# Optimization experiments

Measured on AMD Instinct MI355X. Metric: run time of the kernel, lower is better.

The kernel has to match this reference:

```python
import jax, jax.numpy as jnp
import numpy as np

N = 50000      # nodes
E = 800000     # edges (avg degree 16)
F = 128        # num_features
H = 64         # nhid
S = 3          # num_scatter


def setup_inputs() -> dict:
    key = jax.random.key(0)
    ks = jax.random.split(key, 10)
    x = jax.random.normal(ks[0], (N, F), dtype=jnp.float32)
    scatter_edge_index = jax.random.randint(ks[1], (2, E), 0, N, dtype=jnp.int32)
    scatter_edge_attr = jax.random.normal(ks[2], (E,), dtype=jnp.float32)
    s = 0.05
    lin_W = jax.random.normal(ks[3], (F, H), dtype=jnp.float32) * s
    lin_b = jnp.zeros((H,), dtype=jnp.float32)
    # per-scatter-block 2-layer MLP applied after edge aggregation (layer=2)
    W1 = jax.random.normal(ks[4], (S, H, H), dtype=jnp.float32) * s
    b1 = jnp.zeros((S, H), dtype=jnp.float32)
    W2 = jax.random.normal(ks[5], (S, H, H), dtype=jnp.float32) * s
    b2 = jnp.zeros((S, H), dtype=jnp.float32)
    return {
        'x': x,
        'scatter_edge_index': scatter_edge_index,
        'scatter_edge_attr': scatter_edge_attr,
        'lin_W': lin_W, 'lin_b': lin_b,
        'W1': W1, 'b1': b1, 'W2': W2, 'b2': b2,
    }


def reference(x, scatter_edge_index, scatter_edge_attr, lin_W, lin_b, W1, b1, W2, b2):
    src = scatter_edge_index[0]
    dst = scatter_edge_index[1]
    attr = scatter_edge_attr[:, None]  # [E,1]

    def conv(h, i):
        # gather -> edge-weight -> scatter-add (message passing), then 2-layer MLP
        m = jax.ops.segment_sum(h[src] * attr, dst, num_segments=N)  # [N,H]
        t = jax.nn.relu(m @ W1[i] + b1[i])
        return t @ W2[i] + b2[i]

    h = x @ lin_W + lin_b  # lin_in (dropout is identity at eval)
    outs, scats = [], []
    for i in range(S):
        h = h + conv(h, i)          # residual accumulation
        outs.append(h)
        scats.append(conv(h, i))    # second conv on updated hidden_rep
    return (jnp.stack(scats), jnp.stack(outs))  # ([S,N,H], [S,N,H])
```

## Files before the change

kernel.cpp:

```cpp
#include <hip/hip_runtime.h>

#define NN 50000
#define NE 800000
#define FIN 128
#define HD 64
#define SL 3
#define GBM 782
#define NBIN 196
#define BSH 8
#define CAP 8064

typedef __attribute__((ext_vector_type(8))) short bf16x8;
typedef __attribute__((ext_vector_type(4))) float f32x4;
#define MFMA(A, B, C) __builtin_amdgcn_mfma_f32_16x16x32_bf16(A, B, C, 0, 0, 0)


__device__ __forceinline__ unsigned int bfr(float x) {
    unsigned int u = __float_as_uint(x);
    return (u + 0x7fffu + ((u >> 16) & 1u)) >> 16;
}
__device__ __forceinline__ unsigned int bf2(float lo, float hi) {
    return bfr(lo) | (bfr(hi) << 16);
}


__global__ void zero_k(int* __restrict__ g) {
    if (threadIdx.x < NBIN) g[threadIdx.x] = 0;
}

__global__ __launch_bounds__(256) void binpass_k(const int* __restrict__ src,
                                                 const int* __restrict__ dst,
                                                 const float* __restrict__ attr,
                                                 int* __restrict__ gcur,
                                                 int2* __restrict__ tedge) {
    __shared__ int cnt_lds[256], runbase[256], lcur[256];
    int t = threadIdx.x;
    cnt_lds[t] = 0;
    lcur[t] = 0;
    __syncthreads();
    int base = blockIdx.x * 4096;
    for (int i = t; i < 4096; i += 256) {
        int e = base + i;
        if (e < NE) atomicAdd(&cnt_lds[dst[e] >> BSH], 1);
    }
    __syncthreads();
    if (t < NBIN && cnt_lds[t]) runbase[t] = atomicAdd(&gcur[t], cnt_lds[t]);
    __syncthreads();
    for (int i = t; i < 4096; i += 256) {
        int e = base + i;
        if (e < NE) {
            int d = dst[e];
            int b = d >> BSH;
            int r = atomicAdd(&lcur[b], 1);
            tedge[(size_t)b * CAP + runbase[b] + r] =
                make_int2(src[e] | ((d & 255) << 16), __float_as_int(attr[e]));
        }
    }
}

__global__ __launch_bounds__(256) void binscan_k(const int* __restrict__ gcur,
                                                 int* __restrict__ binoff,
                                                 int* __restrict__ off) {
    __shared__ int sh[256];
    int t = threadIdx.x;
    int v = (t < NBIN) ? gcur[t] : 0;
    sh[t] = v;
    __syncthreads();
    for (int d = 1; d < 256; d <<= 1) {
        int u = (t >= d) ? sh[t - d] : 0;
        __syncthreads();
        sh[t] += u;
        __syncthreads();
    }
    if (t < NBIN) binoff[t] = sh[t] - v;
    if (t == 255) {
        binoff[NBIN] = sh[255];
        off[NN] = sh[255];
    }
}

__global__ __launch_bounds__(256) void sortbin2_k(const int* __restrict__ binoff,
                                                  const int2* __restrict__ tedge,
                                                  int2* __restrict__ cedge,
                                                  int* __restrict__ off) {
    __shared__ int cnt[256], lofs[256], lcur[256];
    int b = blockIdx.x, t = threadIdx.x;
    int s = binoff[b];
    int n_in_bin = binoff[b + 1] - s;
    const int2* tb = tedge + (size_t)b * CAP;
    cnt[t] = 0;
    __syncthreads();
    for (int i = t; i < n_in_bin; i += 256)
        atomicAdd(&cnt[((unsigned)tb[i].x >> 16) & 255], 1);
    __syncthreads();
    int v = cnt[t];
    lofs[t] = v;
    __syncthreads();
    for (int d = 1; d < 256; d <<= 1) {
        int u = (t >= d) ? lofs[t - d] : 0;
        __syncthreads();
        lofs[t] += u;
        __syncthreads();
    }
    int ex = lofs[t] - v;
    int node = (b << BSH) + t;
    if (node < NN) off[node] = s + ex;
    lcur[t] = ex;
    __syncthreads();
    for (int i = t; i < n_in_bin; i += 256) {
        int2 ed = tb[i];
        int dl = ((unsigned)ed.x >> 16) & 255;
        int p = s + atomicAdd(&lcur[dl], 1);
        cedge[p] = make_int2(ed.x & 0xffff, ed.y);
    }
}


__global__ __launch_bounds__(256) void wprep_k(const float* __restrict__ W1,
                                               const float* __restrict__ W2,
                                               const float* __restrict__ linW,
                                               short* __restrict__ prep) {
    int i = blockIdx.x * 256 + threadIdx.x;
    if (i < 24576) {
        int mat = i >> 12;
        int o = i & 4095;
        int j = o & 7, l = (o >> 3) & 63, s = (o >> 9) & 1, t = o >> 10;
        int k = 32 * s + 8 * (l >> 4) + j;
        int n = 16 * t + (l & 15);
        const float* Wsrc = (mat & 1) ? W2 : W1;
        prep[i] = (short)bfr(Wsrc[(mat >> 1) * 4096 + k * 64 + n]);
    } else if (i < 32768) {
        int o = i - 24576;
        int j = o & 7, l = (o >> 3) & 63, s = (o >> 9) & 3, t = o >> 11;
        int k = 32 * s + 8 * (l >> 4) + j;
        int n = 16 * t + (l & 15);
        prep[i] = (short)bfr(linW[k * 64 + n]);
    }
}


__global__ __launch_bounds__(256) void scatter_k(const uint4* __restrict__ hb4,
                                                 const int* __restrict__ off,
                                                 const int2* __restrict__ cedge,
                                                 uint4* __restrict__ mb4) {
    int w    = (blockIdx.x * blockDim.x + threadIdx.x) >> 6;
    int lane = threadIdx.x & 63;
    if (w >= NN) return;
    int g = lane >> 3;
    int f = lane & 7;
    int s = off[w], e = off[w + 1];
    float a0 = 0.f, a1 = 0.f, a2 = 0.f, a3 = 0.f;
    float a4 = 0.f, a5 = 0.f, a6 = 0.f, a7 = 0.f;
    for (int i = s + g; i < e; i += 8) {
        int2 ed = cedge[i];
        uint4 hv = hb4[(size_t)ed.x * 8 + f];
        float a = __int_as_float(ed.y);
        a0 += a * __uint_as_float(hv.x << 16);
        a1 += a * __uint_as_float(hv.x & 0xffff0000u);
        a2 += a * __uint_as_float(hv.y << 16);
        a3 += a * __uint_as_float(hv.y & 0xffff0000u);
        a4 += a * __uint_as_float(hv.z << 16);
        a5 += a * __uint_as_float(hv.z & 0xffff0000u);
        a6 += a * __uint_as_float(hv.w << 16);
        a7 += a * __uint_as_float(hv.w & 0xffff0000u);
    }
#pragma unroll
    for (int msk = 8; msk <= 32; msk <<= 1) {
        a0 += __shfl_xor(a0, msk);
        a1 += __shfl_xor(a1, msk);
        a2 += __shfl_xor(a2, msk);
        a3 += __shfl_xor(a3, msk);
        a4 += __shfl_xor(a4, msk);
        a5 += __shfl_xor(a5, msk);
        a6 += __shfl_xor(a6, msk);
        a7 += __shfl_xor(a7, msk);
    }
    if (g == 0) {
        uint4 o;
        o.x = bf2(a0, a1);
        o.y = bf2(a2, a3);
        o.z = bf2(a4, a5);
        o.w = bf2(a6, a7);
        mb4[(size_t)w * 8 + f] = o;
    }
}


__device__ __forceinline__ void conv_core(bf16x8 a0, bf16x8 a1,
                                          const bf16x8* __restrict__ w1f,
                                          const float* __restrict__ b1,
                                          const bf16x8* __restrict__ w2f,
                                          short* tw, int c, int q, int l,
                                          f32x4 oc[4]) {
    f32x4 acc[4];
#pragma unroll
    for (int t = 0; t < 4; t++) acc[t] = (f32x4){0.f, 0.f, 0.f, 0.f};
#pragma unroll
    for (int t = 0; t < 4; t++) {
        acc[t] = MFMA(a0, w1f[(t * 2 + 0) * 64 + l], acc[t]);
        acc[t] = MFMA(a1, w1f[(t * 2 + 1) * 64 + l], acc[t]);
    }
#pragma unroll
    for (int t = 0; t < 4; t++) {
        float bb = b1[16 * t + c];
#pragma unroll
        for (int rg = 0; rg < 4; rg++) {
            float v = fmaxf(acc[t][rg] + bb, 0.f);
            tw[(4 * q + rg) * 72 + 16 * t + c] = (short)bfr(v);
        }
    }
    __syncthreads();
    bf16x8 ta0 = *(const bf16x8*)&tw[c * 72 + 8 * q];
    bf16x8 ta1 = *(const bf16x8*)&tw[c * 72 + 32 + 8 * q];
#pragma unroll
    for (int t = 0; t < 4; t++) oc[t] = (f32x4){0.f, 0.f, 0.f, 0.f};
#pragma unroll
    for (int t = 0; t < 4; t++) {
        oc[t] = MFMA(ta0, w2f[(t * 2 + 0) * 64 + l], oc[t]);
        oc[t] = MFMA(ta1, w2f[(t * 2 + 1) * 64 + l], oc[t]);
    }
}


template <bool ADD, bool WB>
__global__ __launch_bounds__(256) void convm_k(const unsigned int* __restrict__ mb,
                                               const short* __restrict__ w1p,
                                               const float* __restrict__ b1,
                                               const short* __restrict__ w2p,
                                               const float* __restrict__ b2,
                                               const float* __restrict__ hprev,
                                               float* __restrict__ out,
                                               unsigned int* __restrict__ hb) {
    __shared__ short tls[4][16 * 72];
    int wv = threadIdx.x >> 6, l = threadIdx.x & 63;
    int c = l & 15, q = l >> 4;
    int rbase = blockIdx.x * 64 + wv * 16;

    int ar = rbase + c;
    bool aok = ar < NN;
    uint4 v0 = make_uint4(0, 0, 0, 0), v1 = v0;
    if (aok) {
        const uint4* mp = (const uint4*)(mb + (size_t)ar * 32);
        v0 = mp[q];
        v1 = mp[4 + q];
    }
    bf16x8 a0 = *(bf16x8*)&v0, a1 = *(bf16x8*)&v1;

    f32x4 oc[4];
    conv_core(a0, a1, (const bf16x8*)w1p, b1, (const bf16x8*)w2p, tls[wv], c, q, l, oc);

#pragma unroll
    for (int t = 0; t < 4; t++) {
        float bb = b2[16 * t + c];
#pragma unroll
        for (int rg = 0; rg < 4; rg++) {
            int row = rbase + 4 * q + rg;
            if (row < NN) {
                float v = oc[t][rg] + bb;
                if constexpr (ADD) v += hprev[(size_t)row * 64 + 16 * t + c];
                out[(size_t)row * 64 + 16 * t + c] = v;
                if constexpr (WB) {
                    float o = __shfl_xor(v, 1);
                    if ((c & 1) == 0)
                        hb[(size_t)row * 32 + 8 * t + (c >> 1)] = bf2(v, o);
                }
            }
        }
    }
}


__global__ __launch_bounds__(256) void conv2_k(const unsigned int* __restrict__ mb,
                                               const short* __restrict__ wa1,
                                               const float* __restrict__ ba1,
                                               const short* __restrict__ wa2,
                                               const float* __restrict__ ba2,
                                               const short* __restrict__ wb1,
                                               const float* __restrict__ bb1,
                                               const short* __restrict__ wb2,
                                               const float* __restrict__ bb2,
                                               const float* __restrict__ hprev,
                                               float* __restrict__ outa,
                                               float* __restrict__ outb,
                                               unsigned int* __restrict__ hb) {
    __shared__ short tls[4][16 * 72];
    int wv = threadIdx.x >> 6, l = threadIdx.x & 63;
    int c = l & 15, q = l >> 4;
    int rbase = blockIdx.x * 64 + wv * 16;

    int ar = rbase + c;
    bool aok = ar < NN;
    uint4 v0 = make_uint4(0, 0, 0, 0), v1 = v0;
    if (aok) {
        const uint4* mp = (const uint4*)(mb + (size_t)ar * 32);
        v0 = mp[q];
        v1 = mp[4 + q];
    }
    bf16x8 a0 = *(bf16x8*)&v0, a1 = *(bf16x8*)&v1;

    f32x4 oc[4];
    conv_core(a0, a1, (const bf16x8*)wa1, ba1, (const bf16x8*)wa2, tls[wv], c, q, l, oc);
#pragma unroll
    for (int t = 0; t < 4; t++) {
        float bb = ba2[16 * t + c];
#pragma unroll
        for (int rg = 0; rg < 4; rg++) {
            int row = rbase + 4 * q + rg;
            if (row < NN)
                outa[(size_t)row * 64 + 16 * t + c] = oc[t][rg] + bb;
        }
    }
    __syncthreads();

    conv_core(a0, a1, (const bf16x8*)wb1, bb1, (const bf16x8*)wb2, tls[wv], c, q, l, oc);
#pragma unroll
    for (int t = 0; t < 4; t++) {
        float bb = bb2[16 * t + c];
#pragma unroll
        for (int rg = 0; rg < 4; rg++) {
            int row = rbase + 4 * q + rg;
            if (row < NN) {
                float v = oc[t][rg] + bb + hprev[(size_t)row * 64 + 16 * t + c];
                outb[(size_t)row * 64 + 16 * t + c] = v;
                float o = __shfl_xor(v, 1);
                if ((c & 1) == 0)
                    hb[(size_t)row * 32 + 8 * t + (c >> 1)] = bf2(v, o);
            }
        }
    }
}


__global__ __launch_bounds__(256) void linm_k(const float* __restrict__ x,
                                              const short* __restrict__ wp,
                                              const float* __restrict__ b,
                                              float* __restrict__ h0,
                                              unsigned int* __restrict__ hb) {
    int wv = threadIdx.x >> 6, l = threadIdx.x & 63;
    int c = l & 15, q = l >> 4;
    int rbase = blockIdx.x * 64 + wv * 16;
    int ar = rbase + c;
    bool aok = ar < NN;

    bf16x8 af[4];
#pragma unroll
    for (int s = 0; s < 4; s++) {
        float4 p0 = make_float4(0, 0, 0, 0), p1 = p0;
        if (aok) {
            const float4* xp = (const float4*)(x + (size_t)ar * FIN + 32 * s + 8 * q);
            p0 = xp[0];
            p1 = xp[1];
        }
        bf16x8 t;
        t[0] = (short)bfr(p0.x); t[1] = (short)bfr(p0.y);
        t[2] = (short)bfr(p0.z); t[3] = (short)bfr(p0.w);
        t[4] = (short)bfr(p1.x); t[5] = (short)bfr(p1.y);
        t[6] = (short)bfr(p1.z); t[7] = (short)bfr(p1.w);
        af[s] = t;
    }

    const bf16x8* wf = (const bf16x8*)wp;
    f32x4 acc[4];
#pragma unroll
    for (int t = 0; t < 4; t++) acc[t] = (f32x4){0.f, 0.f, 0.f, 0.f};
#pragma unroll
    for (int t = 0; t < 4; t++)
#pragma unroll
        for (int s = 0; s < 4; s++)
            acc[t] = MFMA(af[s], wf[(t * 4 + s) * 64 + l], acc[t]);

#pragma unroll
    for (int t = 0; t < 4; t++) {
        float bb = b[16 * t + c];
#pragma unroll
        for (int rg = 0; rg < 4; rg++) {
            int row = rbase + 4 * q + rg;
            if (row < NN) {
                float v = acc[t][rg] + bb;
                h0[(size_t)row * 64 + 16 * t + c] = v;
                float o = __shfl_xor(v, 1);
                if ((c & 1) == 0)
                    hb[(size_t)row * 32 + 8 * t + (c >> 1)] = bf2(v, o);
            }
        }
    }
}


extern "C" void kernel_launch(void* const* d_in, const int* in_sizes, int n_in,
                              void* d_out, int out_size, void* d_ws, size_t ws_size,
                              hipStream_t stream) {
    (void)in_sizes; (void)n_in; (void)out_size; (void)ws_size;

    const float* x    = (const float*)d_in[0];
    const int*   ei   = (const int*)d_in[1];
    const float* attr = (const float*)d_in[2];
    const float* linW = (const float*)d_in[3];
    const float* linb = (const float*)d_in[4];
    const float* W1   = (const float*)d_in[5];
    const float* b1   = (const float*)d_in[6];
    const float* W2   = (const float*)d_in[7];
    const float* b2   = (const float*)d_in[8];
    float* out = (float*)d_out;

    float*        h0     = (float*)d_ws;
    unsigned int* mb     = (unsigned int*)(h0 + (size_t)NN * HD);
    unsigned int* hb     = mb + (size_t)NN * 32;
    int2*         cedge  = (int2*)(hb + (size_t)NN * 32);
    short*        prep   = (short*)(cedge + NE);
    int*          off    = (int*)(prep + 32768);
    int*          gcur   = off + NN + 1;
    int*          binoff = gcur + 256;
    int2*         tedge  = (int2*)h0;

    const int* src = ei;
    const int* dst = ei + NE;

    float* scats = out;
    float* outs  = out + (size_t)SL * NN * HD;

    const size_t NH = (size_t)NN * HD;
    const int WB_ = (NN * 64) / 256;

    const short* w1p0 = prep;
    const short* w2p0 = prep + 4096;
    const short* linp = prep + 24576;

    zero_k<<<1, 256, 0, stream>>>(gcur);
    binpass_k<<<196, 256, 0, stream>>>(src, dst, attr, gcur, tedge);
    binscan_k<<<1, 256, 0, stream>>>(gcur, binoff, off);
    sortbin2_k<<<NBIN, 256, 0, stream>>>(binoff, tedge, cedge, off);
    wprep_k<<<128, 256, 0, stream>>>(W1, W2, linW, prep);

    linm_k<<<GBM, 256, 0, stream>>>(x, linp, linb, h0, hb);

    scatter_k<<<WB_, 256, 0, stream>>>((const uint4*)hb, off, cedge, (uint4*)mb);
    convm_k<true, true><<<GBM, 256, 0, stream>>>(mb, w1p0, b1, w2p0, b2, h0, outs, hb);

    scatter_k<<<WB_, 256, 0, stream>>>((const uint4*)hb, off, cedge, (uint4*)mb);
    conv2_k<<<GBM, 256, 0, stream>>>(mb, w1p0, b1, w2p0, b2,
                                     w1p0 + 8192, b1 + 64, w2p0 + 8192, b2 + 64,
                                     outs, scats, outs + NH, hb);

    scatter_k<<<WB_, 256, 0, stream>>>((const uint4*)hb, off, cedge, (uint4*)mb);
    conv2_k<<<GBM, 256, 0, stream>>>(mb, w1p0 + 8192, b1 + 64, w2p0 + 8192, b2 + 64,
                                     w1p0 + 16384, b1 + 128, w2p0 + 16384, b2 + 128,
                                     outs + NH, scats + NH, outs + 2 * NH, hb);

    scatter_k<<<WB_, 256, 0, stream>>>((const uint4*)hb, off, cedge, (uint4*)mb);
    convm_k<false, false><<<GBM, 256, 0, stream>>>(mb, w1p0 + 16384, b1 + 128,
                                                   w2p0 + 16384, b2 + 128,
                                                   nullptr, scats + 2 * NH, nullptr);
}
```

Baseline: 209.2 us.

## Split bf16 hidden features into two feature-half arrays and merge sort/prep kernels

Result: slower. 257.8 us (+23.3%).

```diff
diff --git a/kernel.cpp b/kernel.cpp
--- a/kernel.cpp
+++ b/kernel.cpp
@@ -9,6 +9,7 @@
 #define NBIN 196
 #define BSH 8
 #define CAP 8064
+#define SCB 25000
 
 typedef __attribute__((ext_vector_type(8))) short bf16x8;
 typedef __attribute__((ext_vector_type(4))) float f32x4;
@@ -58,11 +59,36 @@
     }
 }
 
-__global__ __launch_bounds__(256) void binscan_k(const int* __restrict__ gcur,
-                                                 int* __restrict__ binoff,
-                                                 int* __restrict__ off) {
-    __shared__ int sh[256];
+__global__ __launch_bounds__(256) void sortprep_k(const int* __restrict__ gcur,
+                                                  const int2* __restrict__ tedge,
+                                                  int2* __restrict__ cedge,
+                                                  int* __restrict__ off,
+                                                  const float* __restrict__ W1,
+                                                  const float* __restrict__ W2,
+                                                  const float* __restrict__ linW,
+                                                  short* __restrict__ prep) {
     int t = threadIdx.x;
+    if (blockIdx.x >= NBIN) {
+        int i = (blockIdx.x - NBIN) * 256 + t;
+        if (i < 24576) {
+            int mat = i >> 12;
+            int o = i & 4095;
+            int j = o & 7, l = (o >> 3) & 63, s = (o >> 9) & 1, tt = o >> 10;
+            int k = 32 * s + 8 * (l >> 4) + j;
+            int n = 16 * tt + (l & 15);
+            const float* Wsrc = (mat & 1) ? W2 : W1;
+            prep[i] = (short)bfr(Wsrc[(mat >> 1) * 4096 + k * 64 + n]);
+        } else if (i < 32768) {
+            int o = i - 24576;
+            int j = o & 7, l = (o >> 3) & 63, s = (o >> 9) & 3, tt = o >> 11;
+            int k = 32 * s + 8 * (l >> 4) + j;
+            int n = 16 * tt + (l & 15);
+            prep[i] = (short)bfr(linW[k * 64 + n]);
+        }
+        return;
+    }
+    __shared__ int sh[256], cnt[256], lofs[256], lcur[256];
+    int b = blockIdx.x;
     int v = (t < NBIN) ? gcur[t] : 0;
     sh[t] = v;
     __syncthreads();
@@ -72,29 +98,18 @@
         sh[t] += u;
         __syncthreads();
     }
-    if (t < NBIN) binoff[t] = sh[t] - v;
-    if (t == 255) {
-        binoff[NBIN] = sh[255];
-        off[NN] = sh[255];
-    }
-}
-
-__global__ __launch_bounds__(256) void sortbin2_k(const int* __restrict__ binoff,
-                                                  const int2* __restrict__ tedge,
-                                                  int2* __restrict__ cedge,
-                                                  int* __restrict__ off) {
-    __shared__ int cnt[256], lofs[256], lcur[256];
-    int b = blockIdx.x, t = threadIdx.x;
-    int s = binoff[b];
-    int n_in_bin = binoff[b + 1] - s;
+    int s = (b == 0) ? 0 : sh[b - 1];
+    int n_in_bin = sh[b] - s;
+    if (b == NBIN - 1 && t == 0) off[NN] = sh[NBIN - 1];
+
     const int2* tb = tedge + (size_t)b * CAP;
     cnt[t] = 0;
     __syncthreads();
     for (int i = t; i < n_in_bin; i += 256)
         atomicAdd(&cnt[((unsigned)tb[i].x >> 16) & 255], 1);
     __syncthreads();
-    int v = cnt[t];
-    lofs[t] = v;
+    int cv = cnt[t];
+    lofs[t] = cv;
     __syncthreads();
     for (int d = 1; d < 256; d <<= 1) {
         int u = (t >= d) ? lofs[t - d] : 0;
@@ -102,7 +117,7 @@
         lofs[t] += u;
         __syncthreads();
     }
-    int ex = lofs[t] - v;
+    int ex = lofs[t] - cv;
     int node = (b << BSH) + t;
     if (node < NN) off[node] = s + ex;
     lcur[t] = ex;
@@ -116,44 +131,26 @@
 }
 
 
-__global__ __launch_bounds__(256) void wprep_k(const float* __restrict__ W1,
-                                               const float* __restrict__ W2,
-                                               const float* __restrict__ linW,
-                                               short* __restrict__ prep) {
-    int i = blockIdx.x * 256 + threadIdx.x;
-    if (i < 24576) {
-        int mat = i >> 12;
-        int o = i & 4095;
-        int j = o & 7, l = (o >> 3) & 63, s = (o >> 9) & 1, t = o >> 10;
-        int k = 32 * s + 8 * (l >> 4) + j;
-        int n = 16 * t + (l & 15);
-        const float* Wsrc = (mat & 1) ? W2 : W1;
-        prep[i] = (short)bfr(Wsrc[(mat >> 1) * 4096 + k * 64 + n]);
-    } else if (i < 32768) {
-        int o = i - 24576;
-        int j = o & 7, l = (o >> 3) & 63, s = (o >> 9) & 3, t = o >> 11;
-        int k = 32 * s + 8 * (l >> 4) + j;
-        int n = 16 * t + (l & 15);
-        prep[i] = (short)bfr(linW[k * 64 + n]);
-    }
-}
-
-
-__global__ __launch_bounds__(256) void scatter_k(const uint4* __restrict__ hb4,
+__global__ __launch_bounds__(256) void scatter_k(const uint4* __restrict__ hbL,
+                                                 const uint4* __restrict__ hbH,
                                                  const int* __restrict__ off,
                                                  const int2* __restrict__ cedge,
-                                                 uint4* __restrict__ mb4) {
-    int w    = (blockIdx.x * blockDim.x + threadIdx.x) >> 6;
+                                                 uint4* __restrict__ mbL,
+                                                 uint4* __restrict__ mbH) {
+    int gid = blockIdx.x * 4 + (int)(threadIdx.x >> 6);
+    int half = gid >= NN;
+    int w = half ? gid - NN : gid;
+    const uint4* hb4 = half ? hbH : hbL;
+    uint4* mb4 = half ? mbH : mbL;
     int lane = threadIdx.x & 63;
-    if (w >= NN) return;
-    int g = lane >> 3;
-    int f = lane & 7;
+    int g = lane >> 2;
+    int f = lane & 3;
     int s = off[w], e = off[w + 1];
     float a0 = 0.f, a1 = 0.f, a2 = 0.f, a3 = 0.f;
     float a4 = 0.f, a5 = 0.f, a6 = 0.f, a7 = 0.f;
-    for (int i = s + g; i < e; i += 8) {
+    for (int i = s + g; i < e; i += 16) {
         int2 ed = cedge[i];
-        uint4 hv = hb4[(size_t)ed.x * 8 + f];
+        uint4 hv = hb4[(size_t)ed.x * 4 + f];
         float a = __int_as_float(ed.y);
         a0 += a * __uint_as_float(hv.x << 16);
         a1 += a * __uint_as_float(hv.x & 0xffff0000u);
@@ -165,7 +162,7 @@
         a7 += a * __uint_as_float(hv.w & 0xffff0000u);
     }
 #pragma unroll
-    for (int msk = 8; msk <= 32; msk <<= 1) {
+    for (int msk = 4; msk <= 32; msk <<= 1) {
         a0 += __shfl_xor(a0, msk);
         a1 += __shfl_xor(a1, msk);
         a2 += __shfl_xor(a2, msk);
@@ -181,7 +178,7 @@
         o.y = bf2(a2, a3);
         o.z = bf2(a4, a5);
         o.w = bf2(a6, a7);
-        mb4[(size_t)w * 8 + f] = o;
+        mb4[(size_t)w * 4 + f] = o;
     }
 }
 
@@ -222,29 +219,48 @@
 }
 
 
+__device__ __forceinline__ void load_afrag(const uint4* __restrict__ mbL,
+                                           const uint4* __restrict__ mbH,
+                                           int ar, int q, bf16x8& a0, bf16x8& a1) {
+    uint4 v0 = make_uint4(0, 0, 0, 0), v1 = v0;
+    if (ar < NN) {
+        v0 = mbL[(size_t)ar * 4 + q];
+        v1 = mbH[(size_t)ar * 4 + q];
+    }
+    a0 = *(bf16x8*)&v0;
+    a1 = *(bf16x8*)&v1;
+}
+
+
+__device__ __forceinline__ void wb_hb(unsigned int* __restrict__ hbL,
+                                      unsigned int* __restrict__ hbH,
+                                      int row, int t, int c, float v) {
+    float o = __shfl_xor(v, 1);
+    if ((c & 1) == 0) {
+        unsigned int* hx = (t < 2) ? hbL : hbH;
+        hx[(size_t)row * 16 + 8 * (t & 1) + (c >> 1)] = bf2(v, o);
+    }
+}
+
+
 template <bool ADD, bool WB>
-__global__ __launch_bounds__(256) void convm_k(const unsigned int* __restrict__ mb,
+__global__ __launch_bounds__(256) void convm_k(const uint4* __restrict__ mbL,
+                                               const uint4* __restrict__ mbH,
                                                const short* __restrict__ w1p,
                                                const float* __restrict__ b1,
                                                const short* __restrict__ w2p,
                                                const float* __restrict__ b2,
                                                const float* __restrict__ hprev,
                                                float* __restrict__ out,
-                                               unsigned int* __restrict__ hb) {
+                                               unsigned int* __restrict__ hbL,
+                                               unsigned int* __restrict__ hbH) {
     __shared__ short tls[4][16 * 72];
     int wv = threadIdx.x >> 6, l = threadIdx.x & 63;
     int c = l & 15, q = l >> 4;
     int rbase = blockIdx.x * 64 + wv * 16;
 
-    int ar = rbase + c;
-    bool aok = ar < NN;
-    uint4 v0 = make_uint4(0, 0, 0, 0), v1 = v0;
-    if (aok) {
-        const uint4* mp = (const uint4*)(mb + (size_t)ar * 32);
-        v0 = mp[q];
-        v1 = mp[4 + q];
-    }
-    bf16x8 a0 = *(bf16x8*)&v0, a1 = *(bf16x8*)&v1;
+    bf16x8 a0, a1;
+    load_afrag(mbL, mbH, rbase + c, q, a0, a1);
 
     f32x4 oc[4];
     conv_core(a0, a1, (const bf16x8*)w1p, b1, (const bf16x8*)w2p, tls[wv], c, q, l, oc);
@@ -259,18 +275,15 @@
                 float v = oc[t][rg] + bb;
                 if constexpr (ADD) v += hprev[(size_t)row * 64 + 16 * t + c];
                 out[(size_t)row * 64 + 16 * t + c] = v;
-                if constexpr (WB) {
-                    float o = __shfl_xor(v, 1);
-                    if ((c & 1) == 0)
-                        hb[(size_t)row * 32 + 8 * t + (c >> 1)] = bf2(v, o);
-                }
+                if constexpr (WB) wb_hb(hbL, hbH, row, t, c, v);
             }
         }
     }
 }
 
 
-__global__ __launch_bounds__(256) void conv2_k(const unsigned int* __restrict__ mb,
+__global__ __launch_bounds__(256) void conv2_k(const uint4* __restrict__ mbL,
+                                               const uint4* __restrict__ mbH,
                                                const short* __restrict__ wa1,
                                                const float* __restrict__ ba1,
                                                const short* __restrict__ wa2,
@@ -282,21 +295,15 @@
                                                const float* __restrict__ hprev,
                                                float* __restrict__ outa,
                                                float* __restrict__ outb,
-                                               unsigned int* __restrict__ hb) {
+                                               unsigned int* __restrict__ hbL,
+                                               unsigned int* __restrict__ hbH) {
     __shared__ short tls[4][16 * 72];
     int wv = threadIdx.x >> 6, l = threadIdx.x & 63;
     int c = l & 15, q = l >> 4;
     int rbase = blockIdx.x * 64 + wv * 16;
 
-    int ar = rbase + c;
-    bool aok = ar < NN;
-    uint4 v0 = make_uint4(0, 0, 0, 0), v1 = v0;
-    if (aok) {
-        const uint4* mp = (const uint4*)(mb + (size_t)ar * 32);
-        v0 = mp[q];
-        v1 = mp[4 + q];
-    }
-    bf16x8 a0 = *(bf16x8*)&v0, a1 = *(bf16x8*)&v1;
+    bf16x8 a0, a1;
+    load_afrag(mbL, mbH, rbase + c, q, a0, a1);
 
     f32x4 oc[4];
     conv_core(a0, a1, (const bf16x8*)wa1, ba1, (const bf16x8*)wa2, tls[wv], c, q, l, oc);
@@ -322,9 +329,7 @@
             if (row < NN) {
                 float v = oc[t][rg] + bb + hprev[(size_t)row * 64 + 16 * t + c];
                 outb[(size_t)row * 64 + 16 * t + c] = v;
-                float o = __shfl_xor(v, 1);
-                if ((c & 1) == 0)
-                    hb[(size_t)row * 32 + 8 * t + (c >> 1)] = bf2(v, o);
+                wb_hb(hbL, hbH, row, t, c, v);
             }
         }
     }
@@ -335,7 +340,8 @@
                                               const short* __restrict__ wp,
                                               const float* __restrict__ b,
                                               float* __restrict__ h0,
-                                              unsigned int* __restrict__ hb) {
+                                              unsigned int* __restrict__ hbL,
+                                              unsigned int* __restrict__ hbH) {
     int wv = threadIdx.x >> 6, l = threadIdx.x & 63;
     int c = l & 15, q = l >> 4;
     int rbase = blockIdx.x * 64 + wv * 16;
@@ -378,9 +384,7 @@
             if (row < NN) {
                 float v = acc[t][rg] + bb;
                 h0[(size_t)row * 64 + 16 * t + c] = v;
-                float o = __shfl_xor(v, 1);
-                if ((c & 1) == 0)
-                    hb[(size_t)row * 32 + 8 * t + (c >> 1)] = bf2(v, o);
+                wb_hb(hbL, hbH, row, t, c, v);
             }
         }
     }
@@ -404,13 +408,14 @@
     float* out = (float*)d_out;
 
     float*        h0     = (float*)d_ws;
-    unsigned int* mb     = (unsigned int*)(h0 + (size_t)NN * HD);
-    unsigned int* hb     = mb + (size_t)NN * 32;
-    int2*         cedge  = (int2*)(hb + (size_t)NN * 32);
+    unsigned int* mbL    = (unsigned int*)(h0 + (size_t)NN * HD);
+    unsigned int* mbH    = mbL + (size_t)NN * 16;
+    unsigned int* hbL    = mbH + (size_t)NN * 16;
+    unsigned int* hbH    = hbL + (size_t)NN * 16;
+    int2*         cedge  = (int2*)(hbH + (size_t)NN * 16);
     short*        prep   = (short*)(cedge + NE);
     int*          off    = (int*)(prep + 32768);
     int*          gcur   = off + NN + 1;
-    int*          binoff = gcur + 256;
     int2*         tedge  = (int2*)h0;
 
     const int* src = ei;
@@ -420,7 +425,6 @@
     float* outs  = out + (size_t)SL * NN * HD;
 
     const size_t NH = (size_t)NN * HD;
-    const int WB_ = (NN * 64) / 256;
 
     const short* w1p0 = prep;
     const short* w2p0 = prep + 4096;
@@ -428,27 +432,34 @@
 
     zero_k<<<1, 256, 0, stream>>>(gcur);
     binpass_k<<<196, 256, 0, stream>>>(src, dst, attr, gcur, tedge);
-    binscan_k<<<1, 256, 0, stream>>>(gcur, binoff, off);
-    sortbin2_k<<<NBIN, 256, 0, stream>>>(binoff, tedge, cedge, off);
-    wprep_k<<<128, 256, 0, stream>>>(W1, W2, linW, prep);
-
-    linm_k<<<GBM, 256, 0, stream>>>(x, linp, linb, h0, hb);
-
-    scatter_k<<<WB_, 256, 0, stream>>>((const uint4*)hb, off, cedge, (uint4*)mb);
-    convm_k<true, true><<<GBM, 256, 0, stream>>>(mb, w1p0, b1, w2p0, b2, h0, outs, hb);
-
-    scatter_k<<<WB_, 256, 0, stream>>>((const uint4*)hb, off, cedge, (uint4*)mb);
-    conv2_k<<<GBM, 256, 0, stream>>>(mb, w1p0, b1, w2p0, b2,
+    sortprep_k<<<NBIN + 128, 256, 0, stream>>>(gcur, tedge, cedge, off,
+                                               W1, W2, linW, prep);
+
+    linm_k<<<GBM, 256, 0, stream>>>(x, linp, linb, h0, hbL, hbH);
+
+    scatter_k<<<SCB, 256, 0, stream>>>((const uint4*)hbL, (const uint4*)hbH, off, cedge,
+                                       (uint4*)mbL, (uint4*)mbH);
+    convm_k<true, true><<<GBM, 256, 0, stream>>>((const uint4*)mbL, (const uint4*)mbH,
+                                                 w1p0, b1, w2p0, b2, h0, outs, hbL, hbH);
+
+    scatter_k<<<SCB, 256, 0, stream>>>((const uint4*)hbL, (const uint4*)hbH, off, cedge,
+                                       (uint4*)mbL, (uint4*)mbH);
+    conv2_k<<<GBM, 256, 0, stream>>>((const uint4*)mbL, (const uint4*)mbH,
+                                     w1p0, b1, w2p0, b2,
                                      w1p0 + 8192, b1 + 64, w2p0 + 8192, b2 + 64,
-                                     outs, scats, outs + NH, hb);
-
-    scatter_k<<<WB_, 256, 0, stream>>>((const uint4*)hb, off, cedge, (uint4*)mb);
-    conv2_k<<<GBM, 256, 0, stream>>>(mb, w1p0 + 8192, b1 + 64, w2p0 + 8192, b2 + 64,
+                                     outs, scats, outs + NH, hbL, hbH);
+
+    scatter_k<<<SCB, 256, 0, stream>>>((const uint4*)hbL, (const uint4*)hbH, off, cedge,
+                                       (uint4*)mbL, (uint4*)mbH);
+    conv2_k<<<GBM, 256, 0, stream>>>((const uint4*)mbL, (const uint4*)mbH,
+                                     w1p0 + 8192, b1 + 64, w2p0 + 8192, b2 + 64,
                                      w1p0 + 16384, b1 + 128, w2p0 + 16384, b2 + 128,
-                                     outs + NH, scats + NH, outs + 2 * NH, hb);
-
-    scatter_k<<<WB_, 256, 0, stream>>>((const uint4*)hb, off, cedge, (uint4*)mb);
-    convm_k<false, false><<<GBM, 256, 0, stream>>>(mb, w1p0 + 16384, b1 + 128,
+                                     outs + NH, scats + NH, outs + 2 * NH, hbL, hbH);
+
+    scatter_k<<<SCB, 256, 0, stream>>>((const uint4*)hbL, (const uint4*)hbH, off, cedge,
+                                       (uint4*)mbL, (uint4*)mbH);
+    convm_k<false, false><<<GBM, 256, 0, stream>>>((const uint4*)mbL, (const uint4*)mbH,
+                                                   w1p0 + 16384, b1 + 128,
                                                    w2p0 + 16384, b2 + 128,
-                                                   nullptr, scats + 2 * NH, nullptr);
-}
+                                                   nullptr, scats + 2 * NH, nullptr, nullptr);
+}
```

## Fuse bin scan, bin sort and weight prep into one kernel; widen binpass grid

Applied to the files above, without the earlier changes.

Result: slower. 213.4 us (+2.0%).

```diff
diff --git a/kernel.cpp b/kernel.cpp
--- a/kernel.cpp
+++ b/kernel.cpp
@@ -38,15 +38,15 @@
     cnt_lds[t] = 0;
     lcur[t] = 0;
     __syncthreads();
-    int base = blockIdx.x * 4096;
-    for (int i = t; i < 4096; i += 256) {
+    int base = blockIdx.x * 1024;
+    for (int i = t; i < 1024; i += 256) {
         int e = base + i;
         if (e < NE) atomicAdd(&cnt_lds[dst[e] >> BSH], 1);
     }
     __syncthreads();
     if (t < NBIN && cnt_lds[t]) runbase[t] = atomicAdd(&gcur[t], cnt_lds[t]);
     __syncthreads();
-    for (int i = t; i < 4096; i += 256) {
+    for (int i = t; i < 1024; i += 256) {
         int e = base + i;
         if (e < NE) {
             int d = dst[e];
@@ -58,11 +58,36 @@
     }
 }
 
-__global__ __launch_bounds__(256) void binscan_k(const int* __restrict__ gcur,
-                                                 int* __restrict__ binoff,
-                                                 int* __restrict__ off) {
-    __shared__ int sh[256];
+__global__ __launch_bounds__(256) void sortprep_k(const int* __restrict__ gcur,
+                                                  const int2* __restrict__ tedge,
+                                                  int2* __restrict__ cedge,
+                                                  int* __restrict__ off,
+                                                  const float* __restrict__ W1,
+                                                  const float* __restrict__ W2,
+                                                  const float* __restrict__ linW,
+                                                  short* __restrict__ prep) {
     int t = threadIdx.x;
+    if (blockIdx.x >= NBIN) {
+        int i = (blockIdx.x - NBIN) * 256 + t;
+        if (i < 24576) {
+            int mat = i >> 12;
+            int o = i & 4095;
+            int j = o & 7, l = (o >> 3) & 63, s = (o >> 9) & 1, tt = o >> 10;
+            int k = 32 * s + 8 * (l >> 4) + j;
+            int n = 16 * tt + (l & 15);
+            const float* Wsrc = (mat & 1) ? W2 : W1;
+            prep[i] = (short)bfr(Wsrc[(mat >> 1) * 4096 + k * 64 + n]);
+        } else if (i < 32768) {
+            int o = i - 24576;
+            int j = o & 7, l = (o >> 3) & 63, s = (o >> 9) & 3, tt = o >> 11;
+            int k = 32 * s + 8 * (l >> 4) + j;
+            int n = 16 * tt + (l & 15);
+            prep[i] = (short)bfr(linW[k * 64 + n]);
+        }
+        return;
+    }
+    __shared__ int sh[256], cnt[256], lofs[256], lcur[256];
+    int b = blockIdx.x;
     int v = (t < NBIN) ? gcur[t] : 0;
     sh[t] = v;
     __syncthreads();
@@ -72,29 +97,18 @@
         sh[t] += u;
         __syncthreads();
     }
-    if (t < NBIN) binoff[t] = sh[t] - v;
-    if (t == 255) {
-        binoff[NBIN] = sh[255];
-        off[NN] = sh[255];
-    }
-}
-
-__global__ __launch_bounds__(256) void sortbin2_k(const int* __restrict__ binoff,
-                                                  const int2* __restrict__ tedge,
-                                                  int2* __restrict__ cedge,
-                                                  int* __restrict__ off) {
-    __shared__ int cnt[256], lofs[256], lcur[256];
-    int b = blockIdx.x, t = threadIdx.x;
-    int s = binoff[b];
-    int n_in_bin = binoff[b + 1] - s;
+    int s = (b == 0) ? 0 : sh[b - 1];
+    int n_in_bin = sh[b] - s;
+    if (b == NBIN - 1 && t == 0) off[NN] = sh[NBIN - 1];
+
     const int2* tb = tedge + (size_t)b * CAP;
     cnt[t] = 0;
     __syncthreads();
     for (int i = t; i < n_in_bin; i += 256)
         atomicAdd(&cnt[((unsigned)tb[i].x >> 16) & 255], 1);
     __syncthreads();
-    int v = cnt[t];
-    lofs[t] = v;
+    int cv = cnt[t];
+    lofs[t] = cv;
     __syncthreads();
     for (int d = 1; d < 256; d <<= 1) {
         int u = (t >= d) ? lofs[t - d] : 0;
@@ -102,7 +116,7 @@
         lofs[t] += u;
         __syncthreads();
     }
-    int ex = lofs[t] - v;
+    int ex = lofs[t] - cv;
     int node = (b << BSH) + t;
     if (node < NN) off[node] = s + ex;
     lcur[t] = ex;
@@ -112,29 +126,6 @@
         int dl = ((unsigned)ed.x >> 16) & 255;
         int p = s + atomicAdd(&lcur[dl], 1);
         cedge[p] = make_int2(ed.x & 0xffff, ed.y);
-    }
-}
-
-
-__global__ __launch_bounds__(256) void wprep_k(const float* __restrict__ W1,
-                                               const float* __restrict__ W2,
-                                               const float* __restrict__ linW,
-                                               short* __restrict__ prep) {
-    int i = blockIdx.x * 256 + threadIdx.x;
-    if (i < 24576) {
-        int mat = i >> 12;
-        int o = i & 4095;
-        int j = o & 7, l = (o >> 3) & 63, s = (o >> 9) & 1, t = o >> 10;
-        int k = 32 * s + 8 * (l >> 4) + j;
-        int n = 16 * t + (l & 15);
-        const float* Wsrc = (mat & 1) ? W2 : W1;
-        prep[i] = (short)bfr(Wsrc[(mat >> 1) * 4096 + k * 64 + n]);
-    } else if (i < 32768) {
-        int o = i - 24576;
-        int j = o & 7, l = (o >> 3) & 63, s = (o >> 9) & 3, t = o >> 11;
-        int k = 32 * s + 8 * (l >> 4) + j;
-        int n = 16 * t + (l & 15);
-        prep[i] = (short)bfr(linW[k * 64 + n]);
     }
 }
 
@@ -410,7 +401,6 @@
     short*        prep   = (short*)(cedge + NE);
     int*          off    = (int*)(prep + 32768);
     int*          gcur   = off + NN + 1;
-    int*          binoff = gcur + 256;
     int2*         tedge  = (int2*)h0;
 
     const int* src = ei;
@@ -427,10 +417,9 @@
     const short* linp = prep + 24576;
 
     zero_k<<<1, 256, 0, stream>>>(gcur);
-    binpass_k<<<196, 256, 0, stream>>>(src, dst, attr, gcur, tedge);
-    binscan_k<<<1, 256, 0, stream>>>(gcur, binoff, off);
-    sortbin2_k<<<NBIN, 256, 0, stream>>>(binoff, tedge, cedge, off);
-    wprep_k<<<128, 256, 0, stream>>>(W1, W2, linW, prep);
+    binpass_k<<<782, 256, 0, stream>>>(src, dst, attr, gcur, tedge);
+    sortprep_k<<<NBIN + 128, 256, 0, stream>>>(gcur, tedge, cedge, off,
+                                               W1, W2, linW, prep);
 
     linm_k<<<GBM, 256, 0, stream>>>(x, linp, linb, h0, hb);
 
```
